# Kernel tuning notes

Measured on AMD Instinct MI355X. Metric: run time of the kernel, lower is better.

The kernel has to match this reference:

```python
import jax, jax.numpy as jnp
import numpy as np

INF = 1e8
CLIP = 10.0  # clip_logits
H = 128      # hidden/embedding units
D = 3        # embed_dim


def _lstm_cell(x, h, c, Wih, Whh, b):
    # torch LSTM gate order: i, f, g, o
    g = x @ Wih.T + h @ Whh.T + b
    i, f, gg, o = jnp.split(g, 4, axis=-1)
    c = jax.nn.sigmoid(f) * c + jax.nn.sigmoid(i) * jnp.tanh(gg)
    h = jax.nn.sigmoid(o) * jnp.tanh(c)
    return h, c


def setup_inputs() -> dict:
    key = jax.random.key(0)
    ks = jax.random.split(key, 20)
    B, N = 2048, 128
    u = lambda k, shape: jax.random.uniform(k, shape, jnp.float32, -0.08, 0.08)
    return {
        "x": jax.random.normal(ks[0], (B, N, D), jnp.float32),
        "W_embed": u(ks[1], (H, D)),
        "enc_Wih": u(ks[2], (4 * H, H)), "enc_Whh": u(ks[3], (4 * H, H)), "enc_b": u(ks[4], (4 * H,)),
        "dec_Wih": u(ks[5], (4 * H, H)), "dec_Whh": u(ks[6], (4 * H, H)), "dec_b": u(ks[7], (4 * H,)),
        "Wq": u(ks[8], (H, H)), "bq": u(ks[9], (H,)),
        "Wq2": u(ks[10], (H, H)), "bq2": u(ks[11], (H,)),
        "Wref": u(ks[12], (H, H)), "bref": u(ks[13], (H,)),
        "Wref2": u(ks[14], (H, H)), "bref2": u(ks[15], (H,)),
        "Vec": u(ks[16], (H,)), "Vec2": u(ks[17], (H,)),
        "dec_input0": u(ks[18], (H,)),
    }


def reference(x, W_embed, enc_Wih, enc_Whh, enc_b, dec_Wih, dec_Whh, dec_b,
              Wq, bq, Wq2, bq2, Wref, bref, Wref2, bref2, Vec, Vec2, dec_input0):
    B, N, _ = x.shape
    embed = x @ W_embed.T  # (B, N, H)

    # --- Encoder LSTM over the N view points ---
    h0 = jnp.zeros((B, H), x.dtype)
    def enc_step(carry, xt):
        h, c = carry
        h, c = _lstm_cell(xt, h, c, enc_Wih, enc_Whh, enc_b)
        return (h, c), h
    (h, c), hs = jax.lax.scan(enc_step, (h0, h0), jnp.swapaxes(embed, 0, 1))
    ref = jnp.swapaxes(hs, 0, 1)  # (B, N, H) == encoder_h

    # W_ref / W_ref2 are 1x1 convs over a fixed reference -> precompute once
    u2g = ref @ Wref.T + bref    # (B, N, H)
    u2p = ref @ Wref2.T + bref2  # (B, N, H)

    keys = jax.random.split(jax.random.key(42), N)
    mask0 = jnp.zeros((B, N), x.dtype)
    dec_in0 = jnp.broadcast_to(dec_input0, (B, H))

    def dec_step(carry, key):
        h, c, mask, dec_in = carry
        h, c = _lstm_cell(dec_in, h, c, dec_Wih, dec_Whh, dec_b)
        # --- glimpse (num_glimpse = 1) ---
        u1 = h @ Wq.T + bq  # (B, H)
        sc = jnp.einsum('bnh,h->bn', jnp.tanh(u1[:, None, :] + u2g), Vec) - INF * mask
        a = jax.nn.softmax(sc, axis=1)
        q = jnp.einsum('bnh,bn->bh', u2g, a)
        # --- pointer ---
        u1p = q @ Wq2.T + bq2
        logits = jnp.einsum('bnh,h->bn', CLIP * jnp.tanh(u1p[:, None, :] + u2p), Vec2) - INF * mask
        log_p = jax.nn.log_softmax(logits, axis=-1)  # softmax_T = 1
        nxt = jax.random.categorical(key, log_p, axis=-1)  # multinomial sample
        dec_in = jnp.take_along_axis(embed, nxt[:, None, None], axis=1)[:, 0, :]
        mask = mask + jax.nn.one_hot(nxt, N, dtype=mask.dtype)
        return (h, c, mask, dec_in), (nxt, log_p)

    _, (PI_t, logp_t) = jax.lax.scan(dec_step, (h, c, mask0, dec_in0), keys)
    PI = jnp.swapaxes(PI_t, 0, 1)        # (B, N)
    log_ps = jnp.swapaxes(logp_t, 0, 1)  # (B, N, N)
    ll = jnp.take_along_axis(log_ps, PI[:, :, None], axis=2)[..., 0].sum(axis=1)
    return PI, ll
```

## Files before the change

### kernel.cpp

```cpp
#include <hip/hip_runtime.h>
#include <cstdint>
#include <cstddef>


__device__ __forceinline__ float keepf(float v){ asm volatile("" : "+v"(v)); return v; }

__device__ __forceinline__ float xtanh(float x){
  float ax = fabsf(x);
  float xc = fminf(fmaxf(x, -7.90531110763549805f), 7.90531110763549805f);
  float x2 = xc * xc;
  float np = -2.76076847742355e-16f;
  np = fmaf(np, x2, 2.00018790482477e-13f);
  np = fmaf(np, x2, -8.60467152213735e-11f);
  np = fmaf(np, x2, 5.12229709037114e-08f);
  np = fmaf(np, x2, 1.48572235717979e-05f);
  np = fmaf(np, x2, 6.37261928875436e-04f);
  np = fmaf(np, x2, 4.89352455891786e-03f);
  float num = xc * np;
  float dp = 1.19825839466702e-06f;
  dp = fmaf(dp, x2, 1.18534705686654e-04f);
  dp = fmaf(dp, x2, 2.26843463243900e-03f);
  dp = fmaf(dp, x2, 4.89352518554385e-03f);
  float r = num / dp;
  return (ax < 0.0004f) ? x : r;
}

__device__ __forceinline__ float xsig(float x){ return 1.0f / (1.0f + expf(-x)); }

__device__ __forceinline__ void tf2x32(uint32_t k0, uint32_t k1, uint32_t x0, uint32_t x1,
                                       uint32_t& o0, uint32_t& o1){
  const uint32_t ks2 = k0 ^ k1 ^ 0x1BD11BDAu;
  x0 += k0; x1 += k1;
#define RR(r) { x0 += x1; x1 = (x1<<(r))|(x1>>(32-(r))); x1 ^= x0; }
  RR(13) RR(15) RR(26) RR(6)  x0 += k1;  x1 += ks2 + 1u;
  RR(17) RR(29) RR(16) RR(24) x0 += ks2; x1 += k0 + 2u;
  RR(13) RR(15) RR(26) RR(6)  x0 += k0;  x1 += k1 + 3u;
  RR(17) RR(29) RR(16) RR(24) x0 += k1;  x1 += ks2 + 4u;
  RR(13) RR(15) RR(26) RR(6)  x0 += ks2; x1 += k0 + 5u;
#undef RR
  o0 = x0; o1 = x1;
}

__device__ __forceinline__ float gumbel_from(uint32_t k0, uint32_t k1, uint32_t ctr){
  uint32_t a, b; tf2x32(k0, k1, 0u, ctr, a, b);
  uint32_t bits = a ^ b;
  float f = __uint_as_float((bits >> 9) | 0x3F800000u) - 1.0f;
  if (f == 0.0f) f = 1.17549435e-38f;
  return -logf(-logf(f));
}

__global__ void setup_kernel(const float* __restrict__ We, const float* __restrict__ eWih,
                             const float* __restrict__ dWih, const float* __restrict__ dec0,
                             float* __restrict__ M3e, float* __restrict__ M3d, float* __restrict__ g0d){
  int id = blockIdx.x * 256 + threadIdx.x;
  if (id < 1536){
    int oo = id / 3, d = id % 3;
    double a = 0.0;
    for (int k = 0; k < 128; ++k) a += (double)eWih[oo*128+k] * (double)We[k*3+d];
    M3e[oo*4+d] = (float)a;
    if (d == 0) M3e[oo*4+3] = 0.f;
  } else if (id < 3072){
    int id2 = id - 1536; int oo = id2 / 3, d = id2 % 3;
    double a = 0.0;
    for (int k = 0; k < 128; ++k) a += (double)dWih[oo*128+k] * (double)We[k*3+d];
    M3d[oo*4+d] = (float)a;
    if (d == 0) M3d[oo*4+3] = 0.f;
  } else if (id < 3584){
    int oo = id - 3072;
    double a = 0.0;
    for (int k = 0; k < 128; ++k) a += (double)dWih[oo*128+k] * (double)dec0[k];
    g0d[oo] = (float)a;
  }
}

__global__ __launch_bounds__(512, 2) void enc_kernel(
    const float* __restrict__ x, const float* __restrict__ Whh,
    const float* __restrict__ eb, const float* __restrict__ M3,
    float* __restrict__ ref, float* __restrict__ hcfin){
  __shared__ float pred[4][8][512];
  __shared__ float hT[128][8];
  __shared__ float cT[8][128];
  __shared__ float m3s[512][4];
  __shared__ float bs[512];
  __shared__ float xs[8][4];
  const int tid = threadIdx.x;
  const int lane = tid & 63;
  const int b0 = blockIdx.x << 3;

  { int i = tid; bs[i] = eb[i];
    float4 mv = *(const float4*)&M3[i*4]; *(float4*)&m3s[i][0] = mv; }
  for (int i = tid; i < 1024; i += 512){ ((float*)hT)[i] = 0.f; ((float*)cT)[i] = 0.f; }

  const int og = tid & 127, kp = tid >> 7;
  float w[4][32];
#pragma unroll
  for (int c = 0; c < 4; ++c)
#pragma unroll
    for (int i = 0; i < 32; i += 4){
      float4 v = *(const float4*)&Whh[(og*4+c)*128 + kp*32 + i];
      w[c][i] = v.x; w[c][i+1] = v.y; w[c][i+2] = v.z; w[c][i+3] = v.w;
    }
  __syncthreads();

#pragma unroll 1
  for (int t = 0; t < 128; ++t){
    if (tid < 32){ int r = tid >> 2, d = tid & 3;
      xs[r][d] = (d < 3) ? x[((b0+r)*128 + t)*3 + d] : 0.f; }
    float h8[8];
    { int krow = kp*32 + (lane & 31);
      float4 p0 = *(const float4*)&hT[krow][0];
      float4 p1 = *(const float4*)&hT[krow][4];
      h8[0]=p0.x; h8[1]=p0.y; h8[2]=p0.z; h8[3]=p0.w;
      h8[4]=p1.x; h8[5]=p1.y; h8[6]=p1.z; h8[7]=p1.w; }
    float acc[8][4];
#pragma unroll
    for (int r = 0; r < 8; ++r){ acc[r][0]=0.f; acc[r][1]=0.f; acc[r][2]=0.f; acc[r][3]=0.f; }
#pragma unroll
    for (int i = 0; i < 32; ++i){
#pragma unroll
      for (int r = 0; r < 8; ++r){
        float hv = __int_as_float(__builtin_amdgcn_readlane(__float_as_int(h8[r]), i));
        acc[r][0] = fmaf(hv, w[0][i], acc[r][0]);
        acc[r][1] = fmaf(hv, w[1][i], acc[r][1]);
        acc[r][2] = fmaf(hv, w[2][i], acc[r][2]);
        acc[r][3] = fmaf(hv, w[3][i], acc[r][3]);
      }
    }
#pragma unroll
    for (int r = 0; r < 8; ++r){
      float4 v = {acc[r][0], acc[r][1], acc[r][2], acc[r][3]};
      *(float4*)&pred[kp][r][og*4] = v;
    }
    __syncthreads();
    { const int u = tid & 127; const int r0v = (tid >> 7) * 2;
#pragma unroll
      for (int rr = r0v; rr < r0v + 2; ++rr){
        float g[4];
#pragma unroll
        for (int gi = 0; gi < 4; ++gi){
          int oo = u + (gi << 7);
          float hw = ((pred[0][rr][oo] + pred[1][rr][oo]) + pred[2][rr][oo]) + pred[3][rr][oo];
          float xw = fmaf(m3s[oo][2], xs[rr][2], fmaf(m3s[oo][1], xs[rr][1], m3s[oo][0]*xs[rr][0]));
          g[gi] = (xw + hw) + bs[oo];
        }
        float i_ = xsig(g[0]), f_ = xsig(g[1]), gg = xtanh(g[2]), o_ = xsig(g[3]);
        float a1 = keepf(f_ * cT[rr][u]);
        float a2 = keepf(i_ * gg);
        float cn = a1 + a2;
        float hn = o_ * xtanh(cn);
        cT[rr][u] = cn; hT[u][rr] = hn;
        ref[(((size_t)(b0+rr))*128 + t)*128 + u] = hn;
        if (t == 127){ hcfin[(b0+rr)*256 + u] = hn; hcfin[(b0+rr)*256 + 128 + u] = cn; }
      }
    }
    __syncthreads();
  }
}

__global__ __launch_bounds__(512, 2) void dec_kernel(
    const float* __restrict__ x,
    const float* __restrict__ Whh, const float* __restrict__ db,
    const float* __restrict__ Wq, const float* __restrict__ bq,
    const float* __restrict__ Wq2, const float* __restrict__ bq2,
    const float* __restrict__ Wref, const float* __restrict__ bref,
    const float* __restrict__ Wref2, const float* __restrict__ bref2,
    const float* __restrict__ Vec, const float* __restrict__ Vec2,
    const float* __restrict__ M3, const float* __restrict__ g0,
    const float* __restrict__ ref, const float* __restrict__ hcfin,
    float* __restrict__ out){
  __shared__ float u2g[128][132];
  __shared__ float u2p[128][132];
  __shared__ float gbuf[512];
  __shared__ float qpart[16][128];
  __shared__ float hbuf[128], cbuf[128], u1b[128], u1pb[128], qbuf[128];
  __shared__ float scb[128], lpb[128], maskf[128], abuf[128];
  __shared__ float vecb[128], vec2b[128], bqb[128], bq2b[128];
  __shared__ uint32_t keyx[128], keyy[128];
  __shared__ float xrb[4];
  const int tid = threadIdx.x;
  const int lane = tid & 63;
  const int wv = tid >> 6;
  const int b = blockIdx.x;

  if (tid < 128){
    uint32_t a, bb; tf2x32(0u, 42u, 0u, (uint32_t)tid, a, bb);
    keyx[tid] = a; keyy[tid] = bb;
    hbuf[tid] = hcfin[b*256 + tid];
    cbuf[tid] = hcfin[b*256 + 128 + tid];
    maskf[tid] = 0.f;
    vecb[tid] = Vec[tid]; vec2b[tid] = Vec2[tid];
    bqb[tid] = bq[tid];   bq2b[tid] = bq2[tid];
  }
  {
    const int j = tid & 127, m = (tid >> 7) & 1, th = tid >> 8;
    const float* W = m ? Wref2 : Wref;
    const float bj = m ? bref2[j] : bref[j];
    float wrow[128];
#pragma unroll
    for (int k = 0; k < 128; k += 4){ float4 v = *(const float4*)&W[j*128+k];
      wrow[k]=v.x; wrow[k+1]=v.y; wrow[k+2]=v.z; wrow[k+3]=v.w; }
    float* dst = m ? &u2p[0][0] : &u2g[0][0];
#pragma unroll 1
    for (int t = th*64; t < th*64 + 64; ++t){
      const float* rr = ref + (((size_t)b)*128 + t)*128;
      float a = 0.f;
#pragma unroll
      for (int k = 0; k < 128; ++k) a = fmaf(wrow[k], rr[k], a);
      dst[t*132 + j] = a + bj;
    }
  }
  const int o = tid;
  float whh[128];
#pragma unroll
  for (int k = 0; k < 128; k += 4){ float4 v = *(const float4*)&Whh[o*128+k];
    whh[k]=v.x; whh[k+1]=v.y; whh[k+2]=v.z; whh[k+3]=v.w; }
  const float bo = db[o];
  float4 m4 = *(const float4*)&M3[o*4];
  const float g0o = g0[o];
  float llacc = 0.f;
  __syncthreads();

#pragma unroll 1
  for (int t = 0; t < 128; ++t){
    {
      float h0v = hbuf[lane], h1v = hbuf[64+lane];
      float acc = 0.f;
#pragma unroll
      for (int k = 0; k < 64; ++k){
        float hv = __int_as_float(__builtin_amdgcn_readlane(__float_as_int(h0v), k));
        acc = fmaf(hv, whh[k], acc);
      }
#pragma unroll
      for (int k = 0; k < 64; ++k){
        float hv = __int_as_float(__builtin_amdgcn_readlane(__float_as_int(h1v), k));
        acc = fmaf(hv, whh[64+k], acc);
      }
      float xw = (t == 0) ? g0o : fmaf(m4.z, xrb[2], fmaf(m4.y, xrb[1], m4.x*xrb[0]));
      gbuf[o] = (xw + acc) + bo;
    }
    __syncthreads();
    if (tid < 128){
      float gi = gbuf[tid], gf = gbuf[128+tid], gg = gbuf[256+tid], go = gbuf[384+tid];
      float i_ = xsig(gi), f_ = xsig(gf), g_ = xtanh(gg), o_ = xsig(go);
      float a1 = keepf(f_ * cbuf[tid]);
      float a2 = keepf(i_ * g_);
      float cn = a1 + a2;
      float hn = o_ * xtanh(cn);
      cbuf[tid] = cn; hbuf[tid] = hn;
    }
    __syncthreads();
    {
      const int j = tid >> 2, kp = tid & 3;
      float a = 0.f;
#pragma unroll
      for (int i = 0; i < 32; i += 4){
        float4 wv = *(const float4*)&Wq[j*128 + kp*32 + i];
        float4 hv = *(const float4*)&hbuf[kp*32 + i];
        a = fmaf(wv.x,hv.x,a); a = fmaf(wv.y,hv.y,a); a = fmaf(wv.z,hv.z,a); a = fmaf(wv.w,hv.w,a);
      }
      a += __shfl_xor(a, 1);
      a += __shfl_xor(a, 2);
      if (kp == 0) u1b[j] = a + bqb[j];
    }
    __syncthreads();
    {
      const int n = tid >> 2, hp = tid & 3;
      float s = 0.f;
#pragma unroll
      for (int i = 0; i < 32; i += 4){
        float4 ug = *(const float4*)&u2g[n][hp*32 + i];
        float4 uv = *(const float4*)&u1b[hp*32 + i];
        float4 vv = *(const float4*)&vecb[hp*32 + i];
        s = fmaf(xtanh(uv.x+ug.x), vv.x, s);
        s = fmaf(xtanh(uv.y+ug.y), vv.y, s);
        s = fmaf(xtanh(uv.z+ug.z), vv.z, s);
        s = fmaf(xtanh(uv.w+ug.w), vv.w, s);
      }
      s += __shfl_xor(s, 1);
      s += __shfl_xor(s, 2);
      if (hp == 0){ float mm = keepf(1e8f * maskf[n]); scb[n] = s - mm; }
    }
    __syncthreads();
    {
      float v0 = scb[lane], v1 = scb[64+lane];
      float mx = fmaxf(v0, v1);
#pragma unroll
      for (int d2 = 1; d2 < 64; d2 <<= 1) mx = fmaxf(mx, __shfl_xor(mx, d2));
      float e0 = expf(v0 - mx), e1 = expf(v1 - mx);
      float sm = e0 + e1;
#pragma unroll
      for (int d2 = 1; d2 < 64; d2 <<= 1) sm += __shfl_xor(sm, d2);
      abuf[lane] = e0 / sm;
      abuf[64+lane] = e1 / sm;
    }
    {
      const int hc = tid & 31, np = tid >> 5;
      float q0=0.f,q1=0.f,q2=0.f,q3=0.f;
#pragma unroll
      for (int jj = 0; jj < 8; ++jj){
        int n = np*8 + jj;
        float an = abuf[n];
        float4 ug = *(const float4*)&u2g[n][hc*4];
        q0 = fmaf(an, ug.x, q0); q1 = fmaf(an, ug.y, q1);
        q2 = fmaf(an, ug.z, q2); q3 = fmaf(an, ug.w, q3);
      }
      float4 qv = {q0,q1,q2,q3};
      *(float4*)&qpart[np][hc*4] = qv;
    }
    __syncthreads();
    if (tid < 128){
      float s = qpart[0][tid];
#pragma unroll
      for (int np = 1; np < 16; ++np) s += qpart[np][tid];
      qbuf[tid] = s;
    }
    __syncthreads();
    {
      const int j = tid >> 2, kp = tid & 3;
      float a = 0.f;
#pragma unroll
      for (int i = 0; i < 32; i += 4){
        float4 wv = *(const float4*)&Wq2[j*128 + kp*32 + i];
        float4 hv = *(const float4*)&qbuf[kp*32 + i];
        a = fmaf(wv.x,hv.x,a); a = fmaf(wv.y,hv.y,a); a = fmaf(wv.z,hv.z,a); a = fmaf(wv.w,hv.w,a);
      }
      a += __shfl_xor(a, 1);
      a += __shfl_xor(a, 2);
      if (kp == 0) u1pb[j] = a + bq2b[j];
    }
    __syncthreads();
    {
      const int n = tid >> 2, hp = tid & 3;
      float s = 0.f;
#pragma unroll
      for (int i = 0; i < 32; i += 4){
        float4 ug = *(const float4*)&u2p[n][hp*32 + i];
        float4 uv = *(const float4*)&u1pb[hp*32 + i];
        float4 vv = *(const float4*)&vec2b[hp*32 + i];
        s = fmaf(10.0f*xtanh(uv.x+ug.x), vv.x, s);
        s = fmaf(10.0f*xtanh(uv.y+ug.y), vv.y, s);
        s = fmaf(10.0f*xtanh(uv.z+ug.z), vv.z, s);
        s = fmaf(10.0f*xtanh(uv.w+ug.w), vv.w, s);
      }
      s += __shfl_xor(s, 1);
      s += __shfl_xor(s, 2);
      if (hp == 0){ float mm = keepf(1e8f * maskf[n]); scb[n] = s - mm; }
    }
    __syncthreads();
    if (wv == 0){
      float v0 = scb[lane], v1 = scb[64+lane];
      float mx = fmaxf(v0, v1);
#pragma unroll
      for (int d2 = 1; d2 < 64; d2 <<= 1) mx = fmaxf(mx, __shfl_xor(mx, d2));
      float s0 = v0 - mx, s1 = v1 - mx;
      float e0 = expf(s0), e1 = expf(s1);
      float sm = e0 + e1;
#pragma unroll
      for (int d2 = 1; d2 < 64; d2 <<= 1) sm += __shfl_xor(sm, d2);
      float lz = logf(sm);
      float lp0 = s0 - lz, lp1 = s1 - lz;
      lpb[lane] = lp0; lpb[64+lane] = lp1;
      float gv0 = gumbel_from(keyx[t], keyy[t], (uint32_t)(b*128 + lane));
      float gv1 = gumbel_from(keyx[t], keyy[t], (uint32_t)(b*128 + 64 + lane));
      float val0 = gv0 + lp0, val1 = gv1 + lp1;
      float bv; int bi;
      if (val1 > val0){ bv = val1; bi = 64 + lane; } else { bv = val0; bi = lane; }
#pragma unroll
      for (int d2 = 1; d2 < 64; d2 <<= 1){
        float ov = __shfl_xor(bv, d2);
        int   oi = __shfl_xor(bi, d2);
        if (ov > bv || (ov == bv && oi < bi)){ bv = ov; bi = oi; }
      }
      if (lane == 0){
        out[b*128 + t] = (float)bi;
        llacc += lpb[bi];
        maskf[bi] = 1.f;
      }
      if (lane < 3) xrb[lane] = x[((size_t)(b*128 + bi))*3 + lane];
    }
    __syncthreads();
  }
  if (tid == 0) out[262144 + b] = llacc;
}

extern "C" void kernel_launch(void* const* d_in, const int* in_sizes, int n_in,
                              void* d_out, int out_size, void* d_ws, size_t ws_size,
                              hipStream_t stream){
  (void)in_sizes; (void)n_in; (void)out_size; (void)ws_size;
  const float* x        = (const float*)d_in[0];
  const float* W_embed  = (const float*)d_in[1];
  const float* enc_Wih  = (const float*)d_in[2];
  const float* enc_Whh  = (const float*)d_in[3];
  const float* enc_b    = (const float*)d_in[4];
  const float* dec_Wih  = (const float*)d_in[5];
  const float* dec_Whh  = (const float*)d_in[6];
  const float* dec_b    = (const float*)d_in[7];
  const float* Wq       = (const float*)d_in[8];
  const float* bq       = (const float*)d_in[9];
  const float* Wq2      = (const float*)d_in[10];
  const float* bq2      = (const float*)d_in[11];
  const float* Wref     = (const float*)d_in[12];
  const float* bref     = (const float*)d_in[13];
  const float* Wref2    = (const float*)d_in[14];
  const float* bref2    = (const float*)d_in[15];
  const float* Vec      = (const float*)d_in[16];
  const float* Vec2     = (const float*)d_in[17];
  const float* dec0     = (const float*)d_in[18];
  float* out = (float*)d_out;
  char* ws = (char*)d_ws;
  float* ref   = (float*)(ws);
  float* hcfin = (float*)(ws + 134217728);
  float* M3e   = (float*)(ws + 136314880);
  float* M3d   = (float*)(ws + 136323072);
  float* g0d   = (float*)(ws + 136331264);

  setup_kernel<<<14, 256, 0, stream>>>(W_embed, enc_Wih, dec_Wih, dec0, M3e, M3d, g0d);
  enc_kernel<<<256, 512, 0, stream>>>(x, enc_Whh, enc_b, M3e, ref, hcfin);
  dec_kernel<<<2048, 512, 0, stream>>>(x, dec_Whh, dec_b, Wq, bq, Wq2, bq2,
                                       Wref, bref, Wref2, bref2, Vec, Vec2,
                                       M3d, g0d, ref, hcfin, out);
}
```

Baseline: 17.10 ms.

## Keep u2g/u2p slices in registers and replicate shared vectors to cut bank conflicts

Each thread now loads its 32-element slices of u2g and u2p into registers once, before the decoder loop, so the two per-step tanh-score passes no longer read them from LDS. The u2p shared array is reused as scratch for per-quarter replicated copies of h, u1, q, u1p, Vec and Vec2, padded by 136 floats, so that the four hp lanes read different banks instead of hitting the same ones. Launch bounds drop to one block per CU so the extra 64 registers per thread fit without spilling. The trade-off is lower occupancy in both the encoder and decoder kernels.

```diff
diff --git a/kernel.cpp b/kernel.cpp
--- a/kernel.cpp
+++ b/kernel.cpp
@@ -73,7 +73,7 @@
   }
 }
 
-__global__ __launch_bounds__(512, 2) void enc_kernel(
+__global__ __launch_bounds__(512, 1) void enc_kernel(
     const float* __restrict__ x, const float* __restrict__ Whh,
     const float* __restrict__ eb, const float* __restrict__ M3,
     float* __restrict__ ref, float* __restrict__ hcfin){
@@ -157,7 +157,7 @@
   }
 }
 
-__global__ __launch_bounds__(512, 2) void dec_kernel(
+__global__ __launch_bounds__(512, 1) void dec_kernel(
     const float* __restrict__ x,
     const float* __restrict__ Whh, const float* __restrict__ db,
     const float* __restrict__ Wq, const float* __restrict__ bq,
@@ -168,13 +168,11 @@
     const float* __restrict__ M3, const float* __restrict__ g0,
     const float* __restrict__ ref, const float* __restrict__ hcfin,
     float* __restrict__ out){
-  __shared__ float u2g[128][132];
-  __shared__ float u2p[128][132];
+  __shared__ __align__(16) float u2g[128][132];
+  __shared__ __align__(16) float scratch[16896];
   __shared__ float gbuf[512];
-  __shared__ float qpart[16][128];
-  __shared__ float hbuf[128], cbuf[128], u1b[128], u1pb[128], qbuf[128];
-  __shared__ float scb[128], lpb[128], maskf[128], abuf[128];
-  __shared__ float vecb[128], vec2b[128], bqb[128], bq2b[128];
+  __shared__ float hbuf[128], cbuf[128], scb[128], lpb[128], maskf[128], abuf[128];
+  __shared__ float bqb[128], bq2b[128];
   __shared__ uint32_t keyx[128], keyy[128];
   __shared__ float xrb[4];
   const int tid = threadIdx.x;
@@ -188,7 +186,6 @@
     hbuf[tid] = hcfin[b*256 + tid];
     cbuf[tid] = hcfin[b*256 + 128 + tid];
     maskf[tid] = 0.f;
-    vecb[tid] = Vec[tid]; vec2b[tid] = Vec2[tid];
     bqb[tid] = bq[tid];   bq2b[tid] = bq2[tid];
   }
   {
@@ -199,7 +196,7 @@
 #pragma unroll
     for (int k = 0; k < 128; k += 4){ float4 v = *(const float4*)&W[j*128+k];
       wrow[k]=v.x; wrow[k+1]=v.y; wrow[k+2]=v.z; wrow[k+3]=v.w; }
-    float* dst = m ? &u2p[0][0] : &u2g[0][0];
+    float* dst = m ? scratch : &u2g[0][0];
 #pragma unroll 1
     for (int t = th*64; t < th*64 + 64; ++t){
       const float* rr = ref + (((size_t)b)*128 + t)*128;
@@ -209,6 +206,33 @@
       dst[t*132 + j] = a + bj;
     }
   }
+  __syncthreads();
+
+  const int n_ = tid >> 2, hp = tid & 3;
+  float u2gs[32], u2ps[32];
+#pragma unroll
+  for (int i = 0; i < 32; i += 4){
+    float4 g4 = *(const float4*)&u2g[n_][hp*32 + i];
+    u2gs[i]=g4.x; u2gs[i+1]=g4.y; u2gs[i+2]=g4.z; u2gs[i+3]=g4.w;
+    float4 p4 = *(const float4*)&scratch[n_*132 + hp*32 + i];
+    u2ps[i]=p4.x; u2ps[i+1]=p4.y; u2ps[i+2]=p4.z; u2ps[i+3]=p4.w;
+  }
+  __syncthreads();
+
+  float* hrep   = scratch;
+  float* u1rep  = scratch + 544;
+  float* qrep   = scratch + 1088;
+  float* u1prep = scratch + 1632;
+  float* vrep   = scratch + 2176;
+  float* v2rep  = scratch + 2720;
+  float* qpart  = scratch + 3264;
+
+  if (tid < 128){
+    float v1 = Vec[tid], v2 = Vec2[tid];
+#pragma unroll
+    for (int r = 0; r < 4; ++r){ vrep[r*136+tid] = v1; v2rep[r*136+tid] = v2; }
+  }
+
   const int o = tid;
   float whh[128];
 #pragma unroll
@@ -247,38 +271,41 @@
       float cn = a1 + a2;
       float hn = o_ * xtanh(cn);
       cbuf[tid] = cn; hbuf[tid] = hn;
+#pragma unroll
+      for (int r = 0; r < 4; ++r) hrep[r*136 + tid] = hn;
     }
     __syncthreads();
     {
       const int j = tid >> 2, kp = tid & 3;
+      const float* hb = hrep + kp*136;
       float a = 0.f;
 #pragma unroll
       for (int i = 0; i < 32; i += 4){
-        float4 wv = *(const float4*)&Wq[j*128 + kp*32 + i];
-        float4 hv = *(const float4*)&hbuf[kp*32 + i];
-        a = fmaf(wv.x,hv.x,a); a = fmaf(wv.y,hv.y,a); a = fmaf(wv.z,hv.z,a); a = fmaf(wv.w,hv.w,a);
+        float4 wv4 = *(const float4*)&Wq[j*128 + kp*32 + i];
+        float4 hv4 = *(const float4*)&hb[kp*32 + i];
+        a = fmaf(wv4.x,hv4.x,a); a = fmaf(wv4.y,hv4.y,a); a = fmaf(wv4.z,hv4.z,a); a = fmaf(wv4.w,hv4.w,a);
       }
       a += __shfl_xor(a, 1);
       a += __shfl_xor(a, 2);
-      if (kp == 0) u1b[j] = a + bqb[j];
-    }
-    __syncthreads();
-    {
-      const int n = tid >> 2, hp = tid & 3;
+      u1rep[kp*136 + j] = a + bqb[j];
+    }
+    __syncthreads();
+    {
+      const float* ub = u1rep + hp*136 + hp*32;
+      const float* vb = vrep  + hp*136 + hp*32;
       float s = 0.f;
 #pragma unroll
       for (int i = 0; i < 32; i += 4){
-        float4 ug = *(const float4*)&u2g[n][hp*32 + i];
-        float4 uv = *(const float4*)&u1b[hp*32 + i];
-        float4 vv = *(const float4*)&vecb[hp*32 + i];
-        s = fmaf(xtanh(uv.x+ug.x), vv.x, s);
-        s = fmaf(xtanh(uv.y+ug.y), vv.y, s);
-        s = fmaf(xtanh(uv.z+ug.z), vv.z, s);
-        s = fmaf(xtanh(uv.w+ug.w), vv.w, s);
+        float4 uv = *(const float4*)&ub[i];
+        float4 vv = *(const float4*)&vb[i];
+        s = fmaf(xtanh(uv.x+u2gs[i]),   vv.x, s);
+        s = fmaf(xtanh(uv.y+u2gs[i+1]), vv.y, s);
+        s = fmaf(xtanh(uv.z+u2gs[i+2]), vv.z, s);
+        s = fmaf(xtanh(uv.w+u2gs[i+3]), vv.w, s);
       }
       s += __shfl_xor(s, 1);
       s += __shfl_xor(s, 2);
-      if (hp == 0){ float mm = keepf(1e8f * maskf[n]); scb[n] = s - mm; }
+      if (hp == 0){ float mm = keepf(1e8f * maskf[n_]); scb[n_] = s - mm; }
     }
     __syncthreads();
     {
@@ -305,46 +332,48 @@
         q2 = fmaf(an, ug.z, q2); q3 = fmaf(an, ug.w, q3);
       }
       float4 qv = {q0,q1,q2,q3};
-      *(float4*)&qpart[np][hc*4] = qv;
+      *(float4*)&qpart[np*128 + hc*4] = qv;
     }
     __syncthreads();
     if (tid < 128){
-      float s = qpart[0][tid];
-#pragma unroll
-      for (int np = 1; np < 16; ++np) s += qpart[np][tid];
-      qbuf[tid] = s;
+      float s = qpart[tid];
+#pragma unroll
+      for (int np = 1; np < 16; ++np) s += qpart[np*128 + tid];
+#pragma unroll
+      for (int r = 0; r < 4; ++r) qrep[r*136 + tid] = s;
     }
     __syncthreads();
     {
       const int j = tid >> 2, kp = tid & 3;
+      const float* qb = qrep + kp*136;
       float a = 0.f;
 #pragma unroll
       for (int i = 0; i < 32; i += 4){
-        float4 wv = *(const float4*)&Wq2[j*128 + kp*32 + i];
-        float4 hv = *(const float4*)&qbuf[kp*32 + i];
-        a = fmaf(wv.x,hv.x,a); a = fmaf(wv.y,hv.y,a); a = fmaf(wv.z,hv.z,a); a = fmaf(wv.w,hv.w,a);
+        float4 wv4 = *(const float4*)&Wq2[j*128 + kp*32 + i];
+        float4 hv4 = *(const float4*)&qb[kp*32 + i];
+        a = fmaf(wv4.x,hv4.x,a); a = fmaf(wv4.y,hv4.y,a); a = fmaf(wv4.z,hv4.z,a); a = fmaf(wv4.w,hv4.w,a);
       }
       a += __shfl_xor(a, 1);
       a += __shfl_xor(a, 2);
-      if (kp == 0) u1pb[j] = a + bq2b[j];
-    }
-    __syncthreads();
-    {
-      const int n = tid >> 2, hp = tid & 3;
+      u1prep[kp*136 + j] = a + bq2b[j];
+    }
+    __syncthreads();
+    {
+      const float* ub = u1prep + hp*136 + hp*32;
+      const float* vb = v2rep  + hp*136 + hp*32;
       float s = 0.f;
 #pragma unroll
       for (int i = 0; i < 32; i += 4){
-        float4 ug = *(const float4*)&u2p[n][hp*32 + i];
-        float4 uv = *(const float4*)&u1pb[hp*32 + i];
-        float4 vv = *(const float4*)&vec2b[hp*32 + i];
-        s = fmaf(10.0f*xtanh(uv.x+ug.x), vv.x, s);
-        s = fmaf(10.0f*xtanh(uv.y+ug.y), vv.y, s);
-        s = fmaf(10.0f*xtanh(uv.z+ug.z), vv.z, s);
-        s = fmaf(10.0f*xtanh(uv.w+ug.w), vv.w, s);
+        float4 uv = *(const float4*)&ub[i];
+        float4 vv = *(const float4*)&vb[i];
+        s = fmaf(10.0f*xtanh(uv.x+u2ps[i]),   vv.x, s);
+        s = fmaf(10.0f*xtanh(uv.y+u2ps[i+1]), vv.y, s);
+        s = fmaf(10.0f*xtanh(uv.z+u2ps[i+2]), vv.z, s);
+        s = fmaf(10.0f*xtanh(uv.w+u2ps[i+3]), vv.w, s);
       }
       s += __shfl_xor(s, 1);
       s += __shfl_xor(s, 2);
-      if (hp == 0){ float mm = keepf(1e8f * maskf[n]); scb[n] = s - mm; }
+      if (hp == 0){ float mm = keepf(1e8f * maskf[n_]); scb[n_] = s - mm; }
     }
     __syncthreads();
     if (wv == 0){
```

After: 18.41 ms. +7.6%, slower.
